# Kernel tuning notes

Measured on AMD Instinct MI355X. Metric: run time of the kernel, lower is better.

## Reference

```python
import jax, jax.numpy as jnp
import numpy as np
import math

B, L, D, H = 16, 144, 512, 8
DH = D // H          # 64, equals structure feature dim
DS, HS = 64, 8       # structure sub-attention model dim / heads
DFF = 2048

def ln(x, g, b, eps=1e-6):
    m = jnp.mean(x, -1, keepdims=True)
    v = jnp.mean((x - m) ** 2, -1, keepdims=True)
    return (x - m) * jax.lax.rsqrt(v + eps) * g + b

def setup_inputs():
    key = jax.random.key(0)
    ks = iter(jax.random.split(key, 32))
    def w(shape, s=0.02):
        return jax.random.normal(next(ks), shape, jnp.float32) * s
    return {
        "inputs": jax.random.normal(next(ks), (B, L, D), jnp.float32),
        "structure": jax.random.normal(next(ks), (L * L, 4, B, DS), jnp.float32),
        "mask": jax.random.randint(next(ks), (B, L, L), 0, 2, jnp.int32),
        "g_att": jnp.ones((D,), jnp.float32), "b_att": jnp.zeros((D,), jnp.float32),
        "Wq": w((D, D)), "bq": jnp.zeros((D,), jnp.float32),
        "Wk": w((D, D)), "bk": jnp.zeros((D,), jnp.float32),
        "Wv": w((D, D)), "bv": jnp.zeros((D,), jnp.float32),
        "Wo": w((D, D)), "bo": jnp.zeros((D,), jnp.float32),
        "sWq": w((DS, DS)), "sbq": jnp.zeros((DS,), jnp.float32),
        "sWk": w((DS, DS)), "sbk": jnp.zeros((DS,), jnp.float32),
        "sWv": w((DS, DS)), "sbv": jnp.zeros((DS,), jnp.float32),
        "sWo": w((DS, DS)), "sbo": jnp.zeros((DS,), jnp.float32),
        "Wc": w((DS, DS, 4)), "bc": jnp.zeros((DS,), jnp.float32),
        "g_s": jnp.ones((DS,), jnp.float32), "b_s": jnp.zeros((DS,), jnp.float32),
        "g_ffn": jnp.ones((D,), jnp.float32), "b_ffn": jnp.zeros((D,), jnp.float32),
        "W1": w((D, DFF)), "b1": jnp.zeros((DFF,), jnp.float32),
        "W2": w((DFF, D)), "b2": jnp.zeros((D,), jnp.float32),
    }

def _forward(inputs, structure, mask, g_att, b_att, Wq, bq, Wk, bk, Wv, bv, Wo, bo,
             sWq, sbq, sWk, sbk, sWv, sbv, sWo, sbo, Wc, bc, g_s, b_s,
             g_ffn, b_ffn, W1, b1, W2, b2):
    x_norm = ln(inputs, g_att, b_att)

    # --- structure pipeline: [L*L,4,B,DS] -> (transpose(0,1),transpose(0,2)) -> [B,L*L,4,DS] -> [N,4,DS]
    N = B * L * L
    s = jnp.transpose(structure, (2, 0, 1, 3)).reshape(N, 4, DS)
    dsh = DS // HS
    def split_s(t):
        return t.reshape(N, 4, HS, dsh).transpose(0, 2, 1, 3)
    q = split_s(s @ sWq + sbq) / math.sqrt(dsh)
    k = split_s(s @ sWk + sbk)
    v = split_s(s @ sWv + sbv)
    attn = jax.nn.softmax(jnp.einsum('nhid,nhjd->nhij', q, k), -1)
    ctx = jnp.einsum('nhij,nhjd->nhid', attn, v).transpose(0, 2, 1, 3).reshape(N, 4, DS)
    sa = ctx @ sWo + sbo                                  # [N,4,DS]
    # Conv1d(64,64,kernel=4) over the length-4 axis (valid -> length 1) + ReLU
    conv = jax.nn.relu(jnp.einsum('ntc,oct->no', sa, Wc) + bc)  # [N,DS]
    R = ln(conv.reshape(B, L, L, DS), g_s, b_s)           # per-pair relation embeddings

    # --- relation-aware self-attention (structure added to keys and values)
    def split_h(t):
        return t.reshape(B, L, H, DH).transpose(0, 2, 1, 3)
    q = split_h(x_norm @ Wq + bq) / math.sqrt(DH)
    k = split_h(x_norm @ Wk + bk)
    v = split_h(x_norm @ Wv + bv)
    scores = jnp.einsum('bhid,bhjd->bhij', q, k) + jnp.einsum('bhid,bijd->bhij', q, R)
    scores = jnp.where(mask[:, None, :, :] != 0, jnp.float32(-1e18), scores)
    attn = jax.nn.softmax(scores, -1)
    ctx = jnp.einsum('bhij,bhjd->bhid', attn, v) + jnp.einsum('bhij,bijd->bhid', attn, R)
    ctx = ctx.transpose(0, 2, 1, 3).reshape(B, L, D)
    x = ctx @ Wo + bo + inputs

    # --- FFN (pre-LN, residual outside)
    h = jax.nn.relu(ln(x, g_ffn, b_ffn) @ W1 + b1)
    return h @ W2 + b2 + x

def reference(inputs, structure, mask, g_att, b_att, Wq, bq, Wk, bk, Wv, bv, Wo, bo,
              sWq, sbq, sWk, sbk, sWv, sbv, sWo, sbo, Wc, bc, g_s, b_s,
              g_ffn, b_ffn, W1, b1, W2, b2):
    return _forward(inputs, structure, mask, g_att, b_att, Wq, bq, Wk, bk, Wv, bv, Wo, bo,
                    sWq, sbq, sWk, sbk, sWv, sbv, sWo, sbo, Wc, bc, g_s, b_s,
                    g_ffn, b_ffn, W1, b1, W2, b2)
```

## Files before the change

kernel.cpp:

```cpp
#include <hip/hip_runtime.h>
#include <math.h>


typedef __bf16 bf16_t;
typedef __bf16 bf16x8 __attribute__((ext_vector_type(8)));
typedef __bf16 bf16x4 __attribute__((ext_vector_type(4)));
typedef __bf16 bf16x2v __attribute__((ext_vector_type(2)));
typedef float f32x4 __attribute__((ext_vector_type(4)));

__global__ __launch_bounds__(256) void transpose_all(
    const float* __restrict__ Wq, const float* __restrict__ Wk,
    const float* __restrict__ Wv, const float* __restrict__ Wo,
    const float* __restrict__ W1, const float* __restrict__ W2,
    bf16_t* __restrict__ WqkvT, bf16_t* __restrict__ WoT,
    bf16_t* __restrict__ W1T, bf16_t* __restrict__ W2T) {
  int bid = blockIdx.x;
  const float* W; bf16_t* WT; int K, N; float scale = 1.f; int tile;
  if (bid < 256)       { W = Wq; WT = WqkvT;            K = 512;  N = 512;  scale = 0.125f; tile = bid; }
  else if (bid < 512)  { W = Wk; WT = WqkvT + 262144;   K = 512;  N = 512;  tile = bid - 256; }
  else if (bid < 768)  { W = Wv; WT = WqkvT + 524288;   K = 512;  N = 512;  tile = bid - 512; }
  else if (bid < 1024) { W = Wo; WT = WoT;              K = 512;  N = 512;  tile = bid - 768; }
  else if (bid < 2048) { W = W1; WT = W1T;              K = 512;  N = 2048; tile = bid - 1024; }
  else                 { W = W2; WT = W2T;              K = 2048; N = 512;  tile = bid - 2048; }
  int ntn = N >> 5;
  int nb = (tile % ntn) * 32, kb = (tile / ntn) * 32;
  __shared__ float t32[32][33];
  int tx = threadIdx.x & 31, ty = threadIdx.x >> 5;
#pragma unroll
  for (int i = ty; i < 32; i += 8) t32[i][tx] = W[(size_t)(kb + i) * N + nb + tx];
  __syncthreads();
#pragma unroll
  for (int i = ty; i < 32; i += 8)
    WT[(size_t)(nb + i) * K + kb + tx] = (__bf16)(t32[tx][i] * scale);
}

__global__ __launch_bounds__(256) void precompute_misc(
    const float* __restrict__ sWq, const float* __restrict__ sWk,
    const float* __restrict__ sWv, const float* __restrict__ sWo,
    const float* __restrict__ sbq, const float* __restrict__ sbk,
    const float* __restrict__ sbv, const float* __restrict__ sbo,
    const float* __restrict__ Wc, const float* __restrict__ bc,
    const float* __restrict__ bq, const float* __restrict__ bk,
    const float* __restrict__ bv, bf16_t* __restrict__ WT3,
    bf16_t* __restrict__ M2T, float* __restrict__ C0,
    float* __restrict__ sbqkv, float* __restrict__ bqkv) {
  int blk = blockIdx.x, tid = threadIdx.x;
  if (blk == 16) {
    const float qs = 0.35355339059327373f;
    for (int idx = tid; idx < 4096; idx += 256) {
      int j = idx >> 6, ic = idx & 63;
      int cj = (j & 7) * 8 + 2 * ((j >> 4) & 3) + ((j >> 3) & 1);
      WT3[idx] = (__bf16)(sWq[ic * 64 + cj] * qs);
      WT3[4096 + idx] = (__bf16)sWk[ic * 64 + cj];
      WT3[8192 + idx] = (__bf16)sWv[ic * 64 + cj];
    }
    if (tid < 64) {
      float s = bc[tid];
      for (int c = 0; c < 64; ++c) {
        float sb = sbo[c];
#pragma unroll
        for (int t = 0; t < 4; ++t) s += sb * Wc[tid * 256 + c * 4 + t];
      }
      C0[tid] = s;
      int cj = (tid & 7) * 8 + 2 * ((tid >> 4) & 3) + ((tid >> 3) & 1);
      sbqkv[tid] = sbq[cj] * qs;
      sbqkv[64 + tid] = sbk[cj];
      sbqkv[128 + tid] = sbv[cj];
    }
  } else if (blk == 17) {
    for (int i = tid; i < 1536; i += 256)
      bqkv[i] = (i < 512) ? bq[i] * 0.125f
                          : ((i < 1024) ? bk[i - 512] : bv[i - 1024]);
  } else {
    int t = blk >> 2;
    int e = (blk & 3) * 16 + (tid >> 4);
    int o4 = (tid & 15) * 4;
    float acc[4] = {0.f, 0.f, 0.f, 0.f};
    for (int c = 0; c < 64; ++c) {
      float a = sWo[e * 64 + c];
#pragma unroll
      for (int j = 0; j < 4; ++j) acc[j] += a * Wc[(o4 + j) * 256 + c * 4 + t];
    }
#pragma unroll
    for (int j = 0; j < 4; ++j)
      M2T[(o4 + j) * 256 + t * 64 + e] = (__bf16)acc[j];
  }
}

__global__ __launch_bounds__(256) void ln512(
    const float* __restrict__ x, const float* __restrict__ g,
    const float* __restrict__ bb, bf16_t* __restrict__ out) {
  int row = blockIdx.x, tid = threadIdx.x;
  const float* xr = x + (size_t)row * 512;
  float2 v = *(const float2*)&xr[tid * 2];
  float s1 = v.x + v.y;
  float s2 = v.x * v.x + v.y * v.y;
#pragma unroll
  for (int m = 32; m >= 1; m >>= 1) {
    s1 += __shfl_xor(s1, m);
    s2 += __shfl_xor(s2, m);
  }
  __shared__ float red[8];
  int wid = tid >> 6;
  if ((tid & 63) == 0) { red[wid * 2] = s1; red[wid * 2 + 1] = s2; }
  __syncthreads();
  s1 = red[0] + red[2] + red[4] + red[6];
  s2 = red[1] + red[3] + red[5] + red[7];
  float mean = s1 * (1.f / 512.f);
  float var = s2 * (1.f / 512.f) - mean * mean;
  float rs = 1.f / sqrtf(var + 1e-6f);
  int c = tid * 2;
  float2 gg = *(const float2*)&g[c];
  float2 bv = *(const float2*)&bb[c];
  bf16x2v o;
  o[0] = (__bf16)((v.x - mean) * rs * gg.x + bv.x);
  o[1] = (__bf16)((v.y - mean) * rs * gg.y + bv.y);
  *(bf16x2v*)&out[(size_t)row * 512 + c] = o;
}

template <int MR>
__global__ __launch_bounds__(256) void gemm_bf16(
    const bf16_t* __restrict__ A, const bf16_t* __restrict__ BT,
    const float* __restrict__ bias, const float* __restrict__ res,
    float* __restrict__ Cf, bf16_t* __restrict__ Cb, int M, int N, int K,
    int relu) {
  constexpr int RT = MR / 64;
  int tid = threadIdx.x;
  int w = tid >> 6, l = tid & 63, l15 = l & 15, l4 = l >> 4;
  int n0 = blockIdx.x * 64, m0 = blockIdx.y * MR;
  const bf16_t* Arow[RT];
#pragma unroll
  for (int rt = 0; rt < RT; ++rt)
    Arow[rt] = A + (size_t)(m0 + (w * RT + rt) * 16 + l15) * K + l4 * 8;
  const bf16_t* Bbase = BT + (size_t)(n0 + l15) * K + l4 * 8;
  f32x4 acc[RT][4];
#pragma unroll
  for (int ct = 0; ct < 4; ++ct) {
    float bv = bias[n0 + ct * 16 + l15];
#pragma unroll
    for (int rt = 0; rt < RT; ++rt) acc[rt][ct] = (f32x4){bv, bv, bv, bv};
  }
#pragma unroll 4
  for (int k0 = 0; k0 < K; k0 += 32) {
    bf16x8 a8[RT];
#pragma unroll
    for (int rt = 0; rt < RT; ++rt) a8[rt] = *(const bf16x8*)(Arow[rt] + k0);
#pragma unroll
    for (int ct = 0; ct < 4; ++ct) {
      bf16x8 b8 = *(const bf16x8*)(Bbase + (size_t)ct * 16 * K + k0);
#pragma unroll
      for (int rt = 0; rt < RT; ++rt)
        acc[rt][ct] =
            __builtin_amdgcn_mfma_f32_16x16x32_bf16(a8[rt], b8, acc[rt][ct], 0, 0, 0);
    }
  }
#pragma unroll
  for (int ct = 0; ct < 4; ++ct) {
    int col = n0 + ct * 16 + l15;
#pragma unroll
    for (int rt = 0; rt < RT; ++rt) {
#pragma unroll
      for (int i = 0; i < 4; ++i) {
        int row = m0 + (w * RT + rt) * 16 + l4 * 4 + i;
        float vv = acc[rt][ct][i];
        if (relu) vv = fmaxf(vv, 0.f);
        if (res) vv += res[(size_t)row * N + col];
        if (Cf) Cf[(size_t)row * N + col] = vv;
        if (Cb) Cb[(size_t)row * N + col] = (__bf16)vv;
      }
    }
  }
}

__global__ __launch_bounds__(256, 2) void struct_mfma(
    const float* __restrict__ S, const bf16_t* __restrict__ WT3,
    const float* __restrict__ sbqkv, const bf16_t* __restrict__ M2T,
    const float* __restrict__ C0, const float* __restrict__ gs,
    const float* __restrict__ bsv, bf16_t* __restrict__ Rout) {
  __shared__ __align__(16) char smem[67584];
  int tid = threadIdx.x;
  int w = tid >> 6, l = tid & 63, l15 = l & 15, l4 = l >> 4;
  int p0 = blockIdx.x * 4;

  bf16x8 wq[4][2], wk[4][2], wv[4][2];
  float biq[4], bik[4], biv[4];
#pragma unroll
  for (int ct = 0; ct < 4; ++ct) {
    int j = ct * 16 + l15;
#pragma unroll
    for (int kb = 0; kb < 2; ++kb) {
      int off = j * 64 + kb * 32 + l4 * 8;
      wq[ct][kb] = *(const bf16x8*)(WT3 + off);
      wk[ct][kb] = *(const bf16x8*)(WT3 + 4096 + off);
      wv[ct][kb] = *(const bf16x8*)(WT3 + 8192 + off);
    }
    biq[ct] = sbqkv[j];
    bik[ct] = sbqkv[64 + j];
    biv[ct] = sbqkv[128 + j];
  }

  {
    int row = tid >> 4;
    int cb0 = (tid & 15) * 16;
    const float* src = S + (size_t)(p0 * 4 + row) * 1024;
    int key = (row & 7) << 4;
#pragma unroll
    for (int i = 0; i < 8; ++i) {
      int colb = cb0 + i * 256;
      int c0 = colb >> 1;
      float4 u0 = *(const float4*)(src + c0);
      float4 u1 = *(const float4*)(src + c0 + 4);
      bf16x8 a;
      a[0] = (__bf16)u0.x; a[1] = (__bf16)u0.y;
      a[2] = (__bf16)u0.z; a[3] = (__bf16)u0.w;
      a[4] = (__bf16)u1.x; a[5] = (__bf16)u1.y;
      a[6] = (__bf16)u1.z; a[7] = (__bf16)u1.w;
      *(bf16x8*)(smem + row * 2048 + (colb ^ key)) = a;
    }
  }
  __syncthreads();

  int pl = l >> 4, h = l & 7, hi = (l >> 3) & 1;
#pragma unroll 1
  for (int r = 0; r < 4; ++r) {
    int b = r * 4 + w;
    int akey = (l15 & 7) << 4;
    int colb0 = b * 128 + l4 * 16;
    bf16x8 af0 = *(const bf16x8*)(smem + l15 * 2048 + (colb0 ^ akey));
    bf16x8 af1 = *(const bf16x8*)(smem + l15 * 2048 + ((colb0 + 64) ^ akey));
    f32x4 aq[4], ak[4], av[4];
#pragma unroll
    for (int ct = 0; ct < 4; ++ct) {
      aq[ct] = (f32x4){biq[ct], biq[ct], biq[ct], biq[ct]};
      ak[ct] = (f32x4){bik[ct], bik[ct], bik[ct], bik[ct]};
      av[ct] = (f32x4){biv[ct], biv[ct], biv[ct], biv[ct]};
    }
#pragma unroll
    for (int ct = 0; ct < 4; ++ct) {
      aq[ct] = __builtin_amdgcn_mfma_f32_16x16x32_bf16(af0, wq[ct][0], aq[ct], 0, 0, 0);
      aq[ct] = __builtin_amdgcn_mfma_f32_16x16x32_bf16(af1, wq[ct][1], aq[ct], 0, 0, 0);
      ak[ct] = __builtin_amdgcn_mfma_f32_16x16x32_bf16(af0, wk[ct][0], ak[ct], 0, 0, 0);
      ak[ct] = __builtin_amdgcn_mfma_f32_16x16x32_bf16(af1, wk[ct][1], ak[ct], 0, 0, 0);
      av[ct] = __builtin_amdgcn_mfma_f32_16x16x32_bf16(af0, wv[ct][0], av[ct], 0, 0, 0);
      av[ct] = __builtin_amdgcn_mfma_f32_16x16x32_bf16(af1, wv[ct][1], av[ct], 0, 0, 0);
    }
    float Sm[4][4];
#pragma unroll
    for (int i2 = 0; i2 < 4; ++i2)
#pragma unroll
      for (int j2 = 0; j2 < 4; ++j2)
        Sm[i2][j2] = aq[0][i2] * ak[0][j2] + aq[1][i2] * ak[1][j2] +
                     aq[2][i2] * ak[2][j2] + aq[3][i2] * ak[3][j2];
#pragma unroll
    for (int i2 = 0; i2 < 4; ++i2)
#pragma unroll
      for (int j2 = 0; j2 < 4; ++j2)
        Sm[i2][j2] += __shfl_xor(Sm[i2][j2], 8);
    float P[4][4], inv[4];
#pragma unroll
    for (int i2 = 0; i2 < 4; ++i2) {
      float rs = 0.f;
#pragma unroll
      for (int j2 = 0; j2 < 4; ++j2) {
        P[i2][j2] = __expf(Sm[i2][j2]);
        rs += P[i2][j2];
      }
      inv[i2] = __builtin_amdgcn_rcpf(rs);
    }
    int unit = r * 16 + w * 4 + pl;
    char* cb = smem + 32768 + unit * 544;
    int ckey = (unit & 7) << 4;
#pragma unroll
    for (int ct = 0; ct < 4; ++ct) {
      int c = h * 8 + 2 * ct + hi;
#pragma unroll
      for (int i2 = 0; i2 < 4; ++i2) {
        float cx = (P[i2][0] * av[ct][0] + P[i2][1] * av[ct][1] +
                    P[i2][2] * av[ct][2] + P[i2][3] * av[ct][3]) * inv[i2];
        *(bf16_t*)(cb + ((i2 * 128 + c * 2) ^ ckey)) = (__bf16)cx;
      }
    }
  }
  __syncthreads();

  float* cvp = (float*)smem;
  {
    bf16x8 ax[8];
    int rkey = (l15 & 7) << 4;
    char* cbase = smem + 32768 + (w * 16 + l15) * 544;
#pragma unroll
    for (int kb = 0; kb < 8; ++kb) {
      int byt = (kb >> 1) * 128 + (kb & 1) * 64 + l4 * 16;
      ax[kb] = *(const bf16x8*)(cbase + (byt ^ rkey));
    }
#pragma unroll 1
    for (int ct = 0; ct < 4; ++ct) {
      int o = ct * 16 + l15;
      float c0v = C0[o];
      f32x4 acc = (f32x4){c0v, c0v, c0v, c0v};
#pragma unroll
      for (int kb = 0; kb < 8; ++kb) {
        bf16x8 mf = *(const bf16x8*)(M2T + o * 256 + kb * 32 + l4 * 8);
        acc = __builtin_amdgcn_mfma_f32_16x16x32_bf16(ax[kb], mf, acc, 0, 0, 0);
      }
#pragma unroll
      for (int i2 = 0; i2 < 4; ++i2)
        cvp[(w * 16 + l4 * 4 + i2) * 68 + o] = fmaxf(acc[i2], 0.f);
    }
  }
  __syncthreads();

  {
    int unit = tid >> 2, ch0 = (tid & 3) * 16;
    const float* cr = cvp + unit * 68 + ch0;
    float4 v0 = *(const float4*)(cr);
    float4 v1 = *(const float4*)(cr + 4);
    float4 v2 = *(const float4*)(cr + 8);
    float4 v3 = *(const float4*)(cr + 12);
    float s1 = v0.x + v0.y + v0.z + v0.w + v1.x + v1.y + v1.z + v1.w +
               v2.x + v2.y + v2.z + v2.w + v3.x + v3.y + v3.z + v3.w;
    float s2 = v0.x * v0.x + v0.y * v0.y + v0.z * v0.z + v0.w * v0.w +
               v1.x * v1.x + v1.y * v1.y + v1.z * v1.z + v1.w * v1.w +
               v2.x * v2.x + v2.y * v2.y + v2.z * v2.z + v2.w * v2.w +
               v3.x * v3.x + v3.y * v3.y + v3.z * v3.z + v3.w * v3.w;
    s1 += __shfl_xor(s1, 1); s1 += __shfl_xor(s1, 2);
    s2 += __shfl_xor(s2, 1); s2 += __shfl_xor(s2, 2);
    float mean = s1 * (1.f / 64.f);
    float var = s2 * (1.f / 64.f) - mean * mean;
    float rstd = 1.f / sqrtf(var + 1e-6f);
    float4 g0 = *(const float4*)&gs[ch0];
    float4 g1 = *(const float4*)&gs[ch0 + 4];
    float4 g2 = *(const float4*)&gs[ch0 + 8];
    float4 g3 = *(const float4*)&gs[ch0 + 12];
    float4 b0 = *(const float4*)&bsv[ch0];
    float4 b1 = *(const float4*)&bsv[ch0 + 4];
    float4 b2 = *(const float4*)&bsv[ch0 + 8];
    float4 b3 = *(const float4*)&bsv[ch0 + 12];
    bf16x8 o0, o1;
    o0[0] = (__bf16)((v0.x - mean) * rstd * g0.x + b0.x);
    o0[1] = (__bf16)((v0.y - mean) * rstd * g0.y + b0.y);
    o0[2] = (__bf16)((v0.z - mean) * rstd * g0.z + b0.z);
    o0[3] = (__bf16)((v0.w - mean) * rstd * g0.w + b0.w);
    o0[4] = (__bf16)((v1.x - mean) * rstd * g1.x + b1.x);
    o0[5] = (__bf16)((v1.y - mean) * rstd * g1.y + b1.y);
    o0[6] = (__bf16)((v1.z - mean) * rstd * g1.z + b1.z);
    o0[7] = (__bf16)((v1.w - mean) * rstd * g1.w + b1.w);
    o1[0] = (__bf16)((v2.x - mean) * rstd * g2.x + b2.x);
    o1[1] = (__bf16)((v2.y - mean) * rstd * g2.y + b2.y);
    o1[2] = (__bf16)((v2.z - mean) * rstd * g2.z + b2.z);
    o1[3] = (__bf16)((v2.w - mean) * rstd * g2.w + b2.w);
    o1[4] = (__bf16)((v3.x - mean) * rstd * g3.x + b3.x);
    o1[5] = (__bf16)((v3.y - mean) * rstd * g3.y + b3.y);
    o1[6] = (__bf16)((v3.z - mean) * rstd * g3.z + b3.z);
    o1[7] = (__bf16)((v3.w - mean) * rstd * g3.w + b3.w);
    int rr = unit >> 4, w2 = (unit >> 2) & 3, pu = unit & 3;
    int b = rr * 4 + w2;
    size_t base = ((size_t)b * 20736 + p0 + pu) * 64 + ch0;
    *(bf16x8*)&Rout[base] = o0;
    *(bf16x8*)&Rout[base + 8] = o1;
  }
}

__global__ __launch_bounds__(256) void attn_main(
    const bf16_t* __restrict__ qkv, const bf16_t* __restrict__ R,
    const int* __restrict__ msk, bf16_t* __restrict__ ctx_out) {
  const int L = 144;
  int blk = blockIdx.x;
  int b = blk / L, i = blk - b * L;
  int tid = threadIdx.x;
  __shared__ float RlT[64][149];
  __shared__ float scl[8][144];
  __shared__ float q8[512];
  const bf16_t* Rrow = R + ((size_t)(b * L + i)) * L * 64;
  for (int idx = tid; idx < 144 * 8; idx += 256) {
    int j = idx >> 3, d8 = (idx & 7) * 8;
    bf16x8 r8 = *(const bf16x8*)&Rrow[(size_t)j * 64 + d8];
#pragma unroll
    for (int e = 0; e < 8; ++e) RlT[d8 + e][j] = (float)r8[e];
  }
  if (tid < 128) {
    bf16x4 q4 = *(const bf16x4*)&qkv[(size_t)(b * L + i) * 1536 + tid * 4];
    float4 qf;
    qf.x = (float)q4[0]; qf.y = (float)q4[1];
    qf.z = (float)q4[2]; qf.w = (float)q4[3];
    *(float4*)&q8[tid * 4] = qf;
  }
  __syncthreads();
  const bf16_t* kb = qkv + (size_t)b * L * 1536 + 512;
  const int* mrow = msk + (size_t)(b * L + i) * 144;
  for (int idx = tid; idx < 8 * 144; idx += 256) {
    int h = idx / 144, j = idx - h * 144;
    const bf16_t* kr = kb + (size_t)j * 1536 + h * 64;
    float s = 0.f;
#pragma unroll
    for (int d0 = 0; d0 < 64; d0 += 8) {
      bf16x8 k8 = *(const bf16x8*)&kr[d0];
      s += q8[h * 64 + d0 + 0] * ((float)k8[0] + RlT[d0 + 0][j]);
      s += q8[h * 64 + d0 + 1] * ((float)k8[1] + RlT[d0 + 1][j]);
      s += q8[h * 64 + d0 + 2] * ((float)k8[2] + RlT[d0 + 2][j]);
      s += q8[h * 64 + d0 + 3] * ((float)k8[3] + RlT[d0 + 3][j]);
      s += q8[h * 64 + d0 + 4] * ((float)k8[4] + RlT[d0 + 4][j]);
      s += q8[h * 64 + d0 + 5] * ((float)k8[5] + RlT[d0 + 5][j]);
      s += q8[h * 64 + d0 + 6] * ((float)k8[6] + RlT[d0 + 6][j]);
      s += q8[h * 64 + d0 + 7] * ((float)k8[7] + RlT[d0 + 7][j]);
    }
    if (mrow[j] != 0) s = -1e18f;
    scl[h][j] = s;
  }
  __syncthreads();
  int h = tid >> 5, l = tid & 31;
  float m = -3.4e38f;
  for (int j = l; j < 144; j += 32) m = fmaxf(m, scl[h][j]);
#pragma unroll
  for (int mm = 16; mm >= 1; mm >>= 1) m = fmaxf(m, __shfl_xor(m, mm));
  float sum = 0.f;
  for (int j = l; j < 144; j += 32) {
    float p = __expf(scl[h][j] - m);
    scl[h][j] = p;
    sum += p;
  }
#pragma unroll
  for (int mm = 16; mm >= 1; mm >>= 1) sum += __shfl_xor(sum, mm);
  float inv = 1.f / sum;
  __syncthreads();
  int d0 = l * 2;
  float a0 = 0.f, a1 = 0.f;
  const bf16_t* vb = qkv + (size_t)b * L * 1536 + 1024 + h * 64 + d0;
  for (int j = 0; j < 144; ++j) {
    float p = scl[h][j];
    bf16x2v vv = *(const bf16x2v*)&vb[(size_t)j * 1536];
    a0 += p * ((float)vv[0] + RlT[d0][j]);
    a1 += p * ((float)vv[1] + RlT[d0 + 1][j]);
  }
  bf16x2v o;
  o[0] = (__bf16)(a0 * inv);
  o[1] = (__bf16)(a1 * inv);
  *(bf16x2v*)&ctx_out[(size_t)(b * L + i) * 512 + h * 64 + d0] = o;
}

extern "C" void kernel_launch(void* const* d_in, const int* in_sizes, int n_in,
                              void* d_out, int out_size, void* d_ws,
                              size_t ws_size, hipStream_t stream) {
  (void)in_sizes; (void)n_in; (void)out_size; (void)ws_size;
  const float* inputs = (const float*)d_in[0];
  const float* structure = (const float*)d_in[1];
  const int* mask = (const int*)d_in[2];
  const float* g_att = (const float*)d_in[3];
  const float* b_att = (const float*)d_in[4];
  const float* Wq = (const float*)d_in[5];
  const float* bq = (const float*)d_in[6];
  const float* Wk = (const float*)d_in[7];
  const float* bk = (const float*)d_in[8];
  const float* Wv = (const float*)d_in[9];
  const float* bv = (const float*)d_in[10];
  const float* Wo = (const float*)d_in[11];
  const float* bo = (const float*)d_in[12];
  const float* sWq = (const float*)d_in[13];
  const float* sbq = (const float*)d_in[14];
  const float* sWk = (const float*)d_in[15];
  const float* sbk = (const float*)d_in[16];
  const float* sWv = (const float*)d_in[17];
  const float* sbv = (const float*)d_in[18];
  const float* sWo = (const float*)d_in[19];
  const float* sbo = (const float*)d_in[20];
  const float* Wc = (const float*)d_in[21];
  const float* bc = (const float*)d_in[22];
  const float* g_s = (const float*)d_in[23];
  const float* b_s = (const float*)d_in[24];
  const float* g_ffn = (const float*)d_in[25];
  const float* b_ffn = (const float*)d_in[26];
  const float* W1 = (const float*)d_in[27];
  const float* b1 = (const float*)d_in[28];
  const float* W2 = (const float*)d_in[29];
  const float* b2 = (const float*)d_in[30];

  char* base = (char*)d_ws;
  bf16_t* Rw = (bf16_t*)base;
  bf16_t* qkvb = (bf16_t*)(base + 42467328);
  float* xw = (float*)(base + 49545216);
  bf16_t* xnb = (bf16_t*)(base + 54263808);
  bf16_t* ctxb = (bf16_t*)(base + 56623104);
  bf16_t* hb = (bf16_t*)(base + 58982400);
  bf16_t* WqkvT = (bf16_t*)(base + 68419584);
  bf16_t* WoT = (bf16_t*)(base + 69992448);
  bf16_t* W1T = (bf16_t*)(base + 70516736);
  bf16_t* W2T = (bf16_t*)(base + 72613888);
  bf16_t* WT3 = (bf16_t*)(base + 74711040);
  bf16_t* M2T = (bf16_t*)(base + 74735616);
  float* C0w = (float*)(base + 74768384);
  float* sbqkv = (float*)(base + 74768640);
  float* bqkv = (float*)(base + 74769408);
  float* out = (float*)d_out;

  transpose_all<<<3072, 256, 0, stream>>>(Wq, Wk, Wv, Wo, W1, W2, WqkvT, WoT,
                                          W1T, W2T);
  precompute_misc<<<18, 256, 0, stream>>>(sWq, sWk, sWv, sWo, sbq, sbk, sbv,
                                          sbo, Wc, bc, bq, bk, bv, WT3, M2T,
                                          C0w, sbqkv, bqkv);
  ln512<<<2304, 256, 0, stream>>>(inputs, g_att, b_att, xnb);
  gemm_bf16<128><<<dim3(24, 18), 256, 0, stream>>>(
      xnb, WqkvT, bqkv, nullptr, nullptr, qkvb, 2304, 1536, 512, 0);
  struct_mfma<<<5184, 256, 0, stream>>>(structure, WT3, sbqkv, M2T, C0w, g_s,
                                        b_s, Rw);
  attn_main<<<2304, 256, 0, stream>>>(qkvb, Rw, mask, ctxb);
  gemm_bf16<64><<<dim3(8, 36), 256, 0, stream>>>(
      ctxb, WoT, bo, inputs, xw, nullptr, 2304, 512, 512, 0);
  ln512<<<2304, 256, 0, stream>>>(xw, g_ffn, b_ffn, xnb);
  gemm_bf16<128><<<dim3(32, 18), 256, 0, stream>>>(
      xnb, W1T, b1, nullptr, nullptr, hb, 2304, 2048, 512, 1);
  gemm_bf16<64><<<dim3(8, 36), 256, 0, stream>>>(
      hb, W2T, b2, xw, out, nullptr, 2304, 512, 2048, 0);
}
```

Baseline: 501.5 us.

## Split attention into MFMA score/softmax kernel and separate MFMA P·V kernel

Replaces the scalar per-row attention kernel with two kernels. The first computes the q·k and q·R scores with bf16 MFMA, applies the mask and softmax, writes the probabilities to global memory, and computes P·R with MFMA into an fp32 temporary. The second kernel, one block per (batch, head, half), computes P·V with MFMA against a transposed V held in shared memory and adds the temporary. The aim is to move the dot products onto matrix cores and to reuse V across query rows, at the cost of an extra launch, a global round-trip for P and the partial context, and bf16 rounding of the probabilities.

```diff
diff --git a/kernel.cpp b/kernel.cpp
--- a/kernel.cpp
+++ b/kernel.cpp
@@ -361,81 +361,192 @@
   }
 }
 
-__global__ __launch_bounds__(256) void attn_main(
+__global__ __launch_bounds__(256) void attn_score(
     const bf16_t* __restrict__ qkv, const bf16_t* __restrict__ R,
-    const int* __restrict__ msk, bf16_t* __restrict__ ctx_out) {
+    const int* __restrict__ msk, bf16_t* __restrict__ Pg,
+    float* __restrict__ ctmp) {
   const int L = 144;
+  __shared__ __align__(16) char smem[51008];
+  bf16_t* qZ = (bf16_t*)smem;
+  bf16_t* qL = (bf16_t*)(smem + 16640);
+  bf16_t* RT = (bf16_t*)(smem + 18944);
+  bf16_t* PL = (bf16_t*)(smem + 40448);
+  float* scl = (float*)(smem + 45824);
+  int* mskL = (int*)(smem + 50432);
+
   int blk = blockIdx.x;
   int b = blk / L, i = blk - b * L;
   int tid = threadIdx.x;
-  __shared__ float RlT[64][149];
-  __shared__ float scl[8][144];
-  __shared__ float q8[512];
-  const bf16_t* Rrow = R + ((size_t)(b * L + i)) * L * 64;
-  for (int idx = tid; idx < 144 * 8; idx += 256) {
+  int bL = b * L;
+
+  bf16x8 z8;
+#pragma unroll
+  for (int e = 0; e < 8; ++e) z8[e] = (__bf16)0.f;
+
+  for (int idx = tid; idx < 1040; idx += 256) {
+    int r = idx / 65, c8 = (idx - r * 65) * 8;
+    *(bf16x8*)&qZ[r * 520 + c8] = z8;
+  }
+  if (tid < 144) {
+    int r = tid / 9, c8 = (tid - r * 9) * 8;
+    *(bf16x8*)&qL[r * 72 + c8] = z8;
+  }
+  for (int idx = tid; idx < 336; idx += 256) {
+    int r = idx / 21, c8 = (idx - r * 21) * 8;
+    *(bf16x8*)&PL[r * 168 + c8] = z8;
+  }
+  if (tid < 192) {
+    int r = tid / 3, c8 = 144 + (tid - (tid / 3) * 3) * 8;
+    *(bf16x8*)&RT[r * 168 + c8] = z8;
+  }
+  if (tid < 144) mskL[tid] = msk[(size_t)(bL + i) * 144 + tid];
+  __syncthreads();
+
+  if (tid < 64) {
+    int h = tid >> 3, d8 = (tid & 7) * 8;
+    bf16x8 q8 = *(const bf16x8*)&qkv[(size_t)(bL + i) * 1536 + h * 64 + d8];
+    *(bf16x8*)&qZ[h * 520 + h * 64 + d8] = q8;
+    *(bf16x8*)&qL[h * 72 + d8] = q8;
+  }
+  for (int idx = tid; idx < 1152; idx += 256) {
     int j = idx >> 3, d8 = (idx & 7) * 8;
-    bf16x8 r8 = *(const bf16x8*)&Rrow[(size_t)j * 64 + d8];
-#pragma unroll
-    for (int e = 0; e < 8; ++e) RlT[d8 + e][j] = (float)r8[e];
-  }
-  if (tid < 128) {
-    bf16x4 q4 = *(const bf16x4*)&qkv[(size_t)(b * L + i) * 1536 + tid * 4];
-    float4 qf;
-    qf.x = (float)q4[0]; qf.y = (float)q4[1];
-    qf.z = (float)q4[2]; qf.w = (float)q4[3];
-    *(float4*)&q8[tid * 4] = qf;
-  }
-  __syncthreads();
-  const bf16_t* kb = qkv + (size_t)b * L * 1536 + 512;
-  const int* mrow = msk + (size_t)(b * L + i) * 144;
-  for (int idx = tid; idx < 8 * 144; idx += 256) {
-    int h = idx / 144, j = idx - h * 144;
-    const bf16_t* kr = kb + (size_t)j * 1536 + h * 64;
-    float s = 0.f;
-#pragma unroll
-    for (int d0 = 0; d0 < 64; d0 += 8) {
-      bf16x8 k8 = *(const bf16x8*)&kr[d0];
-      s += q8[h * 64 + d0 + 0] * ((float)k8[0] + RlT[d0 + 0][j]);
-      s += q8[h * 64 + d0 + 1] * ((float)k8[1] + RlT[d0 + 1][j]);
-      s += q8[h * 64 + d0 + 2] * ((float)k8[2] + RlT[d0 + 2][j]);
-      s += q8[h * 64 + d0 + 3] * ((float)k8[3] + RlT[d0 + 3][j]);
-      s += q8[h * 64 + d0 + 4] * ((float)k8[4] + RlT[d0 + 4][j]);
-      s += q8[h * 64 + d0 + 5] * ((float)k8[5] + RlT[d0 + 5][j]);
-      s += q8[h * 64 + d0 + 6] * ((float)k8[6] + RlT[d0 + 6][j]);
-      s += q8[h * 64 + d0 + 7] * ((float)k8[7] + RlT[d0 + 7][j]);
-    }
-    if (mrow[j] != 0) s = -1e18f;
-    scl[h][j] = s;
-  }
-  __syncthreads();
-  int h = tid >> 5, l = tid & 31;
-  float m = -3.4e38f;
-  for (int j = l; j < 144; j += 32) m = fmaxf(m, scl[h][j]);
-#pragma unroll
-  for (int mm = 16; mm >= 1; mm >>= 1) m = fmaxf(m, __shfl_xor(m, mm));
-  float sum = 0.f;
-  for (int j = l; j < 144; j += 32) {
-    float p = __expf(scl[h][j] - m);
-    scl[h][j] = p;
-    sum += p;
-  }
-#pragma unroll
-  for (int mm = 16; mm >= 1; mm >>= 1) sum += __shfl_xor(sum, mm);
-  float inv = 1.f / sum;
-  __syncthreads();
-  int d0 = l * 2;
-  float a0 = 0.f, a1 = 0.f;
-  const bf16_t* vb = qkv + (size_t)b * L * 1536 + 1024 + h * 64 + d0;
-  for (int j = 0; j < 144; ++j) {
-    float p = scl[h][j];
-    bf16x2v vv = *(const bf16x2v*)&vb[(size_t)j * 1536];
-    a0 += p * ((float)vv[0] + RlT[d0][j]);
-    a1 += p * ((float)vv[1] + RlT[d0 + 1][j]);
-  }
-  bf16x2v o;
-  o[0] = (__bf16)(a0 * inv);
-  o[1] = (__bf16)(a1 * inv);
-  *(bf16x2v*)&ctx_out[(size_t)(b * L + i) * 512 + h * 64 + d0] = o;
+    bf16x8 r8 = *(const bf16x8*)&R[((size_t)(bL + i) * 144 + j) * 64 + d8];
+#pragma unroll
+    for (int e = 0; e < 8; ++e) RT[(d8 + e) * 168 + j] = r8[e];
+  }
+  __syncthreads();
+
+  int w = tid >> 6, l = tid & 63, l15 = l & 15, l4 = l >> 4;
+
+  {
+#pragma unroll 1
+    for (int jt = w; jt < 9; jt += 4) {
+      const bf16_t* kg =
+          qkv + (size_t)(bL + jt * 16 + l15) * 1536 + 512 + l4 * 8;
+      f32x4 acc = (f32x4){0.f, 0.f, 0.f, 0.f};
+#pragma unroll
+      for (int ks = 0; ks < 16; ++ks) {
+        bf16x8 a8 = *(const bf16x8*)&qZ[l15 * 520 + ks * 32 + l4 * 8];
+        bf16x8 b8 = *(const bf16x8*)(kg + ks * 32);
+        acc = __builtin_amdgcn_mfma_f32_16x16x32_bf16(a8, b8, acc, 0, 0, 0);
+      }
+      const bf16_t* rg =
+          R + ((size_t)(bL + i) * 144 + jt * 16 + l15) * 64 + l4 * 8;
+      bf16x8 a0 = *(const bf16x8*)&qL[l15 * 72 + l4 * 8];
+      bf16x8 a1 = *(const bf16x8*)&qL[l15 * 72 + 32 + l4 * 8];
+      acc = __builtin_amdgcn_mfma_f32_16x16x32_bf16(a0, *(const bf16x8*)rg,
+                                                    acc, 0, 0, 0);
+      acc = __builtin_amdgcn_mfma_f32_16x16x32_bf16(
+          a1, *(const bf16x8*)(rg + 32), acc, 0, 0, 0);
+      if (l4 < 2) {
+        int j = jt * 16 + l15;
+        bool mm = mskL[j] != 0;
+#pragma unroll
+        for (int i2 = 0; i2 < 4; ++i2)
+          scl[(l4 * 4 + i2) * 144 + j] = mm ? -1e18f : acc[i2];
+      }
+    }
+  }
+  __syncthreads();
+
+  {
+    int h = tid >> 5, lw = tid & 31;
+    float m = -3.4e38f;
+    for (int j = lw; j < 144; j += 32) m = fmaxf(m, scl[h * 144 + j]);
+#pragma unroll
+    for (int mm = 16; mm >= 1; mm >>= 1) m = fmaxf(m, __shfl_xor(m, mm));
+    float sum = 0.f;
+    for (int j = lw; j < 144; j += 32) {
+      float p = __expf(scl[h * 144 + j] - m);
+      scl[h * 144 + j] = p;
+      sum += p;
+    }
+#pragma unroll
+    for (int mm = 16; mm >= 1; mm >>= 1) sum += __shfl_xor(sum, mm);
+    float inv = 1.f / sum;
+    bf16_t* pgrow = Pg + ((size_t)(b * 8 + h) * 144 + i) * 160;
+    for (int j = lw; j < 144; j += 32) {
+      __bf16 pv = (__bf16)(scl[h * 144 + j] * inv);
+      PL[h * 168 + j] = pv;
+      pgrow[j] = pv;
+    }
+    if (lw < 16) pgrow[144 + lw] = (__bf16)0.f;
+  }
+  __syncthreads();
+
+  {
+    f32x4 acc = (f32x4){0.f, 0.f, 0.f, 0.f};
+#pragma unroll
+    for (int ks = 0; ks < 5; ++ks) {
+      bf16x8 a8 = *(const bf16x8*)&PL[l15 * 168 + ks * 32 + l4 * 8];
+      bf16x8 b8 = *(const bf16x8*)&RT[(w * 16 + l15) * 168 + ks * 32 + l4 * 8];
+      acc = __builtin_amdgcn_mfma_f32_16x16x32_bf16(a8, b8, acc, 0, 0, 0);
+    }
+    if (l4 < 2) {
+      float* crow = ctmp + (size_t)(bL + i) * 512;
+#pragma unroll
+      for (int i2 = 0; i2 < 4; ++i2)
+        crow[(l4 * 4 + i2) * 64 + w * 16 + l15] = acc[i2];
+    }
+  }
+}
+
+__global__ __launch_bounds__(256) void attn_pv(
+    const bf16_t* __restrict__ qkv, const bf16_t* __restrict__ Pg,
+    const float* __restrict__ ctmp, bf16_t* __restrict__ ctx_out) {
+  const int L = 144;
+  __shared__ __align__(16) bf16_t VT[64 * 168];
+  int bx = blockIdx.x;
+  int bh = bx >> 1, half = bx & 1;
+  int b = bh >> 3, h = bh & 7;
+  int tid = threadIdx.x;
+  int bL = b * L;
+
+  bf16x8 z8;
+#pragma unroll
+  for (int e = 0; e < 8; ++e) z8[e] = (__bf16)0.f;
+  for (int idx = tid; idx < 1152; idx += 256) {
+    int j = idx >> 3, d8 = (idx & 7) * 8;
+    bf16x8 v8 =
+        *(const bf16x8*)&qkv[(size_t)(bL + j) * 1536 + 1024 + h * 64 + d8];
+#pragma unroll
+    for (int e = 0; e < 8; ++e) VT[(d8 + e) * 168 + j] = v8[e];
+  }
+  if (tid < 192) {
+    int r = tid / 3, c8 = 144 + (tid - (tid / 3) * 3) * 8;
+    *(bf16x8*)&VT[r * 168 + c8] = z8;
+  }
+  __syncthreads();
+
+  int w = tid >> 6, l = tid & 63, l15 = l & 15, l4 = l >> 4;
+  const bf16_t* pbase = Pg + (size_t)(b * 8 + h) * 144 * 160;
+  int itEnd = half ? 9 : 5;
+#pragma unroll 1
+  for (int it = half * 5 + w; it < itEnd; it += 4) {
+    const bf16_t* arow = pbase + (size_t)(it * 16 + l15) * 160 + l4 * 8;
+    f32x4 acc[4];
+#pragma unroll
+    for (int ct = 0; ct < 4; ++ct) acc[ct] = (f32x4){0.f, 0.f, 0.f, 0.f};
+#pragma unroll
+    for (int ks = 0; ks < 5; ++ks) {
+      bf16x8 a8 = *(const bf16x8*)(arow + ks * 32);
+#pragma unroll
+      for (int ct = 0; ct < 4; ++ct) {
+        bf16x8 b8 =
+            *(const bf16x8*)&VT[(ct * 16 + l15) * 168 + ks * 32 + l4 * 8];
+        acc[ct] = __builtin_amdgcn_mfma_f32_16x16x32_bf16(a8, b8, acc[ct], 0, 0, 0);
+      }
+    }
+#pragma unroll
+    for (int ct = 0; ct < 4; ++ct) {
+#pragma unroll
+      for (int i2 = 0; i2 < 4; ++i2) {
+        int row = it * 16 + l4 * 4 + i2;
+        size_t off = (size_t)(bL + row) * 512 + h * 64 + ct * 16 + l15;
+        ctx_out[off] = (__bf16)(acc[ct][i2] + ctmp[off]);
+      }
+    }
+  }
 }
 
 extern "C" void kernel_launch(void* const* d_in, const int* in_sizes, int n_in,
@@ -490,6 +601,8 @@
   float* C0w = (float*)(base + 74768384);
   float* sbqkv = (float*)(base + 74768640);
   float* bqkv = (float*)(base + 74769408);
+  bf16_t* Pg = hb;
+  float* ctmp = xw;
   float* out = (float*)d_out;
 
   transpose_all<<<3072, 256, 0, stream>>>(Wq, Wk, Wv, Wo, W1, W2, WqkvT, WoT,
@@ -502,7 +615,8 @@
       xnb, WqkvT, bqkv, nullptr, nullptr, qkvb, 2304, 1536, 512, 0);
   struct_mfma<<<5184, 256, 0, stream>>>(structure, WT3, sbqkv, M2T, C0w, g_s,
                                         b_s, Rw);
-  attn_main<<<2304, 256, 0, stream>>>(qkvb, Rw, mask, ctxb);
+  attn_score<<<2304, 256, 0, stream>>>(qkvb, Rw, mask, Pg, ctmp);
+  attn_pv<<<256, 256, 0, stream>>>(qkvb, Pg, ctmp, ctxb);
   gemm_bf16<64><<<dim3(8, 36), 256, 0, stream>>>(
       ctxb, WoT, bo, inputs, xw, nullptr, 2304, 512, 512, 0);
   ln512<<<2304, 256, 0, stream>>>(xw, g_ffn, b_ffn, xnb);
```

Measured after the change: 481.9 us. -3.9%, faster.
